# Kernel tuning notes

Hardware: AMD Instinct MI355X
Metric: run time of the kernel (lower is better)

Reference implementation:

```python
import jax, jax.numpy as jnp
import numpy as np

# BlockShuffle (butterfly) dims for in=4096 -> out=16384, nblocks=16
K, Q, P = 16, 256, 256   # w1: (k, q, p), k*p = n = 4096
L, S, R = 16, 1024, 256  # w2: (l, s, r), l*r = k*q = 4096; out = l*s = 16384
BATCH = 4096


def setup_inputs() -> dict:
    key = jax.random.key(0)
    kx, k1, k2 = jax.random.split(key, 3)
    x = jax.random.normal(kx, (BATCH, K * P), dtype=jnp.float32)
    # xavier-style init: std = fan_in^-0.5 (per _init_weights)
    w1 = jax.random.normal(k1, (K, Q, P), dtype=jnp.float32) * (P ** -0.5)
    w2 = jax.random.normal(k2, (L, S, R), dtype=jnp.float32) * (R ** -0.5)
    return {"x": x, "w1": w1, "w2": w2}


def reference(x, w1, w2):
    bd, n = x.shape
    k, q, p = w1.shape
    l, s, r = w2.shape
    # stage 1: block-diagonal matmul over k blocks of size p -> q
    out1 = jnp.einsum('bkp,kqp->bkq', x.reshape(bd, k, p), w1)  # (bd, k, q)
    # shuffle: view (k*q) as (r, l), transpose -> (l, r) blocks
    out1 = out1.reshape(bd, r, l).transpose(0, 2, 1)            # (bd, l, r)
    # stage 2: block-diagonal matmul over l blocks of size r -> s;
    # torch permute(1,2,0).reshape gives index order i = s_idx * l + l_idx
    out2 = jnp.einsum('blr,lsr->bsl', out1, w2)                 # (bd, s, l)
    return out2.reshape(bd, s * l)
```

## Files before the change

### kernel.cpp

```cpp
#include <hip/hip_runtime.h>

typedef __attribute__((ext_vector_type(8)))  short short8;
typedef __attribute__((ext_vector_type(4)))  short short4v;
typedef __attribute__((ext_vector_type(4)))  float f32x4;
typedef __attribute__((ext_vector_type(16))) float f32x16;

__device__ inline short f2bf(float f) {
  unsigned u = __float_as_uint(f);
  u += 0x7fffu + ((u >> 16) & 1u);
  return (short)(u >> 16);
}

__global__ void cvt_all(const float* __restrict__ w1, short* __restrict__ w1b,
                        const float* __restrict__ w2, short* __restrict__ w2f) {
  if (blockIdx.x < 1024) {
    int i = blockIdx.x * 256 + threadIdx.x;
    f32x4 v = ((const f32x4*)w1)[i];
    short4v o;
    o[0] = f2bf(v[0]); o[1] = f2bf(v[1]); o[2] = f2bf(v[2]); o[3] = f2bf(v[3]);
    ((short4v*)w1b)[i] = o;
    return;
  }
  int t = (blockIdx.x - 1024) * 256 + threadIdx.x;
  int lane  = t & 63;
  int f     = t >> 6;
  int kh    = f & 1;
  int ck    = (f >> 1) & 7;
  int stile = (f >> 4) & 31;
  int l     = f >> 9;
  int lrow = lane & 31, khalf = lane >> 5;
  int s = stile * 32 + lrow;
  int r = ck * 32 + kh * 16 + khalf * 8;
  const float* src = w2 + (size_t)(l * 1024 + s) * 256 + r;
  f32x4 lo = *(const f32x4*)src;
  f32x4 hi = *(const f32x4*)(src + 4);
  short8 o;
  o[0]=f2bf(lo[0]); o[1]=f2bf(lo[1]); o[2]=f2bf(lo[2]); o[3]=f2bf(lo[3]);
  o[4]=f2bf(hi[0]); o[5]=f2bf(hi[1]); o[6]=f2bf(hi[2]); o[7]=f2bf(hi[3]);
  ((short8*)w2f)[t] = o;
}

__global__ __launch_bounds__(256) void stage1_kernel(
    const float* __restrict__ x, const short* __restrict__ w1b, short* __restrict__ interf) {
  __shared__ __align__(16) char smem[65536];
  const int tid  = threadIdx.x;
  const int lane = tid & 63;
  const int wq   = tid >> 6;
  const int b0   = blockIdx.x * 64;
  const int k    = blockIdx.y;
  const int q0w  = wq * 64;
  const int lr   = lane & 15;
  const int kid  = lane >> 4;

  #pragma unroll
  for (int i = 0; i < 16; ++i) {
    int idx = i * 256 + tid;
    int row = idx >> 6, seg = idx & 63;
    f32x4 v = *(const f32x4*)(x + (size_t)(b0 + row) * 4096 + k * 256 + seg * 4);
    int byte = (row * 1024 + seg * 16) ^ ((row & 7) << 4);
    *(f32x4*)(smem + byte) = v;
  }
  __syncthreads();

  f32x4 acc[4][4] = {};
  const short* wbase = w1b + k * 65536 + (q0w + lr) * 256 + kid * 8;

  #pragma unroll
  for (int kk = 0; kk < 256; kk += 32) {
    short8 a[4], b[4];
    #pragma unroll
    for (int mt = 0; mt < 4; ++mt) {
      int row = mt * 16 + lr;
      int u = row * 1024 + kid * 32 + kk * 4;
      int s = (row & 7) << 4;
      f32x4 lo = *(const f32x4*)(smem + (u ^ s));
      f32x4 hi = *(const f32x4*)(smem + ((u + 16) ^ s));
      short8 av;
      av[0] = f2bf(lo[0]); av[1] = f2bf(lo[1]); av[2] = f2bf(lo[2]); av[3] = f2bf(lo[3]);
      av[4] = f2bf(hi[0]); av[5] = f2bf(hi[1]); av[6] = f2bf(hi[2]); av[7] = f2bf(hi[3]);
      a[mt] = av;
    }
    #pragma unroll
    for (int nt = 0; nt < 4; ++nt)
      b[nt] = *(const short8*)(wbase + nt * 16 * 256 + kk);
    #pragma unroll
    for (int mt = 0; mt < 4; ++mt)
      #pragma unroll
      for (int nt = 0; nt < 4; ++nt)
        acc[mt][nt] = __builtin_amdgcn_mfma_f32_16x16x32_bf16(a[mt], b[nt], acc[mt][nt], 0, 0, 0);
  }

  __syncthreads();

  #pragma unroll
  for (int mt = 0; mt < 4; ++mt) {
    #pragma unroll
    for (int j = 0; j < 4; ++j) {
      int blocal = mt * 16 + kid * 4 + j;
      int byte = (blocal * 512 + lr * 32 + wq * 8) ^ ((blocal & 7) << 4);
      short4v v;
      #pragma unroll
      for (int nt = 0; nt < 4; ++nt) v[nt] = f2bf(acc[mt][nt][j]);
      *(short4v*)(smem + byte) = v;
    }
  }
  __syncthreads();

  const int brow = lane & 31, khalf = lane >> 5;
  #pragma unroll
  for (int j = 0; j < 8; ++j) {
    int f   = j * 4 + wq;
    int btl = f >> 4, l = f & 15;
    int blc = btl * 32 + brow;
    int rbyte = (blc * 512 + l * 32 + khalf * 16) ^ ((blc & 7) << 4);
    short8 v = *(const short8*)(smem + rbyte);
    size_t off = (((size_t)(blockIdx.x * 2 + btl) * 16 + l) * 16 + k) * 512 + lane * 8;
    *(short8*)(interf + off) = v;
  }
}

__global__ __launch_bounds__(1024) void stage2_kernel(
    const short* __restrict__ interf, const short* __restrict__ w2f, float* __restrict__ out) {
  __shared__ float clds[16 * 1024];
  const int tid  = threadIdx.x;
  const int lane = tid & 63;
  const int l    = tid >> 6;
  const int lrow = lane & 31;
  const int khalf = lane >> 5;

  const int L    = blockIdx.x;
  const int xcd  = L & 7;
  const int pos  = L >> 3;
  const int pass = pos >> 6;
  const int idx  = pos & 63;
  const int st   = idx >> 2;
  const int bt   = idx & 3;
  const int BBT  = xcd * 8 + pass * 4 + bt;
  const int BST  = st;
  const int b0 = BBT * 64, s0 = BST * 64;

  const short* ap = interf + (size_t)(BBT * 2) * 131072 + l * 8192 + lane * 8;
  const short* bp = w2f + (size_t)l * 262144 + (size_t)(BST * 2) * 8192 + lane * 8;

  f32x16 acc[2][2] = {};

  #pragma unroll
  for (int ks = 0; ks < 16; ++ks) {
    short8 a0 = *(const short8*)(ap + ks * 512);
    short8 a1 = *(const short8*)(ap + 131072 + ks * 512);
    short8 b0 = *(const short8*)(bp + ks * 512);
    short8 b1 = *(const short8*)(bp + 8192 + ks * 512);
    acc[0][0] = __builtin_amdgcn_mfma_f32_32x32x16_bf16(a0, b0, acc[0][0], 0, 0, 0);
    acc[0][1] = __builtin_amdgcn_mfma_f32_32x32x16_bf16(a0, b1, acc[0][1], 0, 0, 0);
    acc[1][0] = __builtin_amdgcn_mfma_f32_32x32x16_bf16(a1, b0, acc[1][0], 0, 0, 0);
    acc[1][1] = __builtin_amdgcn_mfma_f32_32x32x16_bf16(a1, b1, acc[1][1], 0, 0, 0);
  }

  #pragma unroll
  for (int c = 0; c < 4; ++c) {
    const int bt2 = c >> 1, rh = c & 1;
    #pragma unroll
    for (int stt = 0; stt < 2; ++stt) {
      int scol = stt * 32 + lrow;
      #pragma unroll
      for (int rr = 0; rr < 8; ++rr) {
        int row16 = (rr & 3) + 8 * (rr >> 2) + 4 * khalf;
        int colx = scol * 16 + (l ^ ((scol & 3) << 2) ^ (((row16 >> 2) & 3) << 2));
        clds[row16 * 1024 + colx] = acc[bt2][stt][rh * 8 + rr];
      }
    }
    __syncthreads();
    #pragma unroll
    for (int p = 0; p < 4; ++p) {
      int idx2 = p * 1024 + tid;
      int row  = idx2 >> 8;
      int slot = idx2 & 255;
      int scol = slot >> 2, lq = slot & 3;
      int colx = scol * 16 + ((lq * 4) ^ ((scol & 3) << 2) ^ (((row >> 2) & 3) << 2));
      f32x4 v = *(const f32x4*)&clds[row * 1024 + colx];
      *(f32x4*)(out + (size_t)(b0 + c * 16 + row) * 16384
                     + (size_t)(s0 + scol) * 16 + lq * 4) = v;
    }
    __syncthreads();
  }
}

extern "C" void kernel_launch(void* const* d_in, const int* in_sizes, int n_in,
                              void* d_out, int out_size, void* d_ws, size_t ws_size,
                              hipStream_t stream) {
  const float* x  = (const float*)d_in[0];
  const float* w1 = (const float*)d_in[1];
  const float* w2 = (const float*)d_in[2];
  float* out = (float*)d_out;

  short* interf = (short*)d_ws;
  short* w1b    = (short*)((char*)d_ws + (32u << 20));
  short* w2f    = (short*)((char*)d_ws + (34u << 20));

  cvt_all<<<3072, 256, 0, stream>>>(w1, w1b, w2, w2f);
  stage1_kernel<<<dim3(64, 16), 256, 0, stream>>>(x, w1b, interf);
  stage2_kernel<<<1024, 1024, 0, stream>>>(interf, w2f, out);
}
```

Before: 153.4 us.

## Split stage2 blocks across l halves to halve block size and LDS

Stage 2 now launches 2048 blocks of 512 threads, with each block handling 8 of the 16 l-blocks instead of all 16. The LDS staging buffer is halved and uses a simpler unswizzled layout, and each thread gathers four scalars from LDS to form a float4 store. The aim is more resident blocks per CU and better latency hiding. In exchange, output writes become 32-byte segments per row chunk instead of 64-byte ones, and the strided scalar LDS reads may cause bank conflicts.

```diff
diff --git a/kernel.cpp b/kernel.cpp
--- a/kernel.cpp
+++ b/kernel.cpp
@@ -119,18 +119,19 @@
   }
 }
 
-__global__ __launch_bounds__(1024) void stage2_kernel(
+__global__ __launch_bounds__(512, 4) void stage2_kernel(
     const short* __restrict__ interf, const short* __restrict__ w2f, float* __restrict__ out) {
-  __shared__ float clds[16 * 1024];
+  __shared__ float clds[16 * 512];
   const int tid  = threadIdx.x;
   const int lane = tid & 63;
-  const int l    = tid >> 6;
+  const int l8   = tid >> 6;
   const int lrow = lane & 31;
   const int khalf = lane >> 5;
 
   const int L    = blockIdx.x;
-  const int xcd  = L & 7;
-  const int pos  = L >> 3;
+  const int lh   = L & 1;
+  const int xcd  = (L >> 1) & 7;
+  const int pos  = L >> 4;
   const int pass = pos >> 6;
   const int idx  = pos & 63;
   const int st   = idx >> 2;
@@ -138,6 +139,7 @@
   const int BBT  = xcd * 8 + pass * 4 + bt;
   const int BST  = st;
   const int b0 = BBT * 64, s0 = BST * 64;
+  const int l  = lh * 8 + l8;
 
   const short* ap = interf + (size_t)(BBT * 2) * 131072 + l * 8192 + lane * 8;
   const short* bp = w2f + (size_t)l * 262144 + (size_t)(BST * 2) * 8192 + lane * 8;
@@ -148,12 +150,12 @@
   for (int ks = 0; ks < 16; ++ks) {
     short8 a0 = *(const short8*)(ap + ks * 512);
     short8 a1 = *(const short8*)(ap + 131072 + ks * 512);
-    short8 b0 = *(const short8*)(bp + ks * 512);
-    short8 b1 = *(const short8*)(bp + 8192 + ks * 512);
-    acc[0][0] = __builtin_amdgcn_mfma_f32_32x32x16_bf16(a0, b0, acc[0][0], 0, 0, 0);
-    acc[0][1] = __builtin_amdgcn_mfma_f32_32x32x16_bf16(a0, b1, acc[0][1], 0, 0, 0);
-    acc[1][0] = __builtin_amdgcn_mfma_f32_32x32x16_bf16(a1, b0, acc[1][0], 0, 0, 0);
-    acc[1][1] = __builtin_amdgcn_mfma_f32_32x32x16_bf16(a1, b1, acc[1][1], 0, 0, 0);
+    short8 b0v = *(const short8*)(bp + ks * 512);
+    short8 b1v = *(const short8*)(bp + 8192 + ks * 512);
+    acc[0][0] = __builtin_amdgcn_mfma_f32_32x32x16_bf16(a0, b0v, acc[0][0], 0, 0, 0);
+    acc[0][1] = __builtin_amdgcn_mfma_f32_32x32x16_bf16(a0, b1v, acc[0][1], 0, 0, 0);
+    acc[1][0] = __builtin_amdgcn_mfma_f32_32x32x16_bf16(a1, b0v, acc[1][0], 0, 0, 0);
+    acc[1][1] = __builtin_amdgcn_mfma_f32_32x32x16_bf16(a1, b1v, acc[1][1], 0, 0, 0);
   }
 
   #pragma unroll
@@ -165,21 +167,22 @@
       #pragma unroll
       for (int rr = 0; rr < 8; ++rr) {
         int row16 = (rr & 3) + 8 * (rr >> 2) + 4 * khalf;
-        int colx = scol * 16 + (l ^ ((scol & 3) << 2) ^ (((row16 >> 2) & 3) << 2));
-        clds[row16 * 1024 + colx] = acc[bt2][stt][rh * 8 + rr];
+        clds[row16 * 512 + l8 * 64 + scol] = acc[bt2][stt][rh * 8 + rr];
       }
     }
     __syncthreads();
     #pragma unroll
     for (int p = 0; p < 4; ++p) {
-      int idx2 = p * 1024 + tid;
-      int row  = idx2 >> 8;
-      int slot = idx2 & 255;
-      int scol = slot >> 2, lq = slot & 3;
-      int colx = scol * 16 + ((lq * 4) ^ ((scol & 3) << 2) ^ (((row >> 2) & 3) << 2));
-      f32x4 v = *(const f32x4*)&clds[row * 1024 + colx];
+      int idx2 = p * 512 + tid;
+      int row  = idx2 >> 7;
+      int slot = idx2 & 127;
+      int scol = slot >> 1, lq2 = slot & 1;
+      f32x4 v;
+      #pragma unroll
+      for (int i = 0; i < 4; ++i)
+        v[i] = clds[row * 512 + (lq2 * 4 + i) * 64 + scol];
       *(f32x4*)(out + (size_t)(b0 + c * 16 + row) * 16384
-                     + (size_t)(s0 + scol) * 16 + lq * 4) = v;
+                     + (size_t)(s0 + scol) * 16 + lh * 8 + lq2 * 4) = v;
     }
     __syncthreads();
   }
@@ -199,5 +202,5 @@
 
   cvt_all<<<3072, 256, 0, stream>>>(w1, w1b, w2, w2f);
   stage1_kernel<<<dim3(64, 16), 256, 0, stream>>>(x, w1b, interf);
-  stage2_kernel<<<1024, 1024, 0, stream>>>(interf, w2f, out);
-}
+  stage2_kernel<<<2048, 512, 0, stream>>>(interf, w2f, out);
+}
```

Result: slower. 226.4 us (+47.6%).
